# Kernel tuning notes

Hardware: AMD Instinct MI355X
Metric: run time of the kernel (lower is better)

Reference implementation:

```python
import jax, jax.numpy as jnp
import numpy as np

NEG_INF = -1e30  # stand-in for float('-inf') that is softmax-safe


def setup_inputs() -> dict:
    key = jax.random.key(0)
    ks = jax.random.split(key, 6)
    B, H, S, D = 2, 8, 1024, 64
    NF, K = 4, 3
    return {
        "query": jax.random.normal(ks[0], (B, H, S, D), dtype=jnp.float32),
        "keys": jax.random.normal(ks[1], (B, H, S, D), dtype=jnp.float32),
        "vals": jax.random.normal(ks[2], (B, H, S, D), dtype=jnp.float32),
        "mask": jnp.ones((B, 1, S, S), dtype=jnp.int32),
        "conv_w": jax.random.normal(ks[3], (NF, 1, K, K), dtype=jnp.float32) * (1.0 / K),
        "conv_b": jnp.zeros((NF,), dtype=jnp.float32),
        "lin_w": jax.random.normal(ks[4], (1, NF), dtype=jnp.float32) * 0.5,
        "lin_b": jnp.zeros((1,), dtype=jnp.float32),
    }


def reference(query, keys, vals, mask, conv_w, conv_b, lin_w, lin_b):
    B, H, S, D = query.shape
    NF = conv_w.shape[0]
    K = conv_w.shape[2]
    scale = jnp.asarray(D, query.dtype) ** 0.5

    # [B,H,S,S] raw dot-product scores
    dp = jnp.einsum("bhsd,bhtd->bhst", query, keys) / scale

    # conv2d over the score matrix: treat (B*H) as batch, 1 input channel
    x = dp.reshape(B * H, 1, S, S)
    conv = jax.lax.conv_general_dilated(
        x, conv_w,
        window_strides=(1, 1),
        padding=[(K // 2, K // 2), (K // 2, K // 2)],
        dimension_numbers=("NCHW", "OIHW", "NCHW"),
    ) + conv_b[None, :, None, None]
    conv = jax.nn.leaky_relu(conv, negative_slope=0.01)  # [B*H, NF, S, S]

    # per-pixel linear over the filter axis (Linear(num_filters, 1))
    conv = conv.reshape(B, H, NF, S, S)
    preattn = jnp.einsum("bhfst,f->bhst", conv, lin_w[0]) + lin_b[0]

    # masking + softmax (mask broadcasts over heads)
    preattn = jnp.where(mask == 0, jnp.asarray(NEG_INF, preattn.dtype), preattn)
    attn = jax.nn.softmax(preattn, axis=-1)

    # dropout is identity in eval mode
    return jnp.einsum("bhst,bhtd->bhsd", attn, vals)
```

## Files before the change

kernel.cpp:

```cpp
#include <hip/hip_runtime.h>
#include <math.h>

#define S_LEN 1024
#define D_DIM 64
#define NBH   16
#define RPB   14
#define NSB   74

typedef unsigned short ushort_t;
typedef unsigned int uint_t;
typedef __attribute__((ext_vector_type(8))) _Float16 half8;
typedef __attribute__((ext_vector_type(2))) _Float16 h2;
typedef __attribute__((ext_vector_type(4))) short short4v;
typedef __attribute__((ext_vector_type(4))) float f32x4;

__device__ __forceinline__ ushort_t f16bits(float x) {
    _Float16 h = (_Float16)x;
    ushort_t b;
    __builtin_memcpy(&b, &h, 2);
    return b;
}
__device__ __forceinline__ h2 as_h2(uint_t u) {
    h2 r;
    __builtin_memcpy(&r, &u, 4);
    return r;
}
__device__ __forceinline__ float uniform_f(float x) {
    return __int_as_float(__builtin_amdgcn_readfirstlane(__float_as_int(x)));
}
__device__ __forceinline__ float fast_exp2(float x) {
#if __has_builtin(__builtin_amdgcn_exp2f)
    return __builtin_amdgcn_exp2f(x);
#else
    return exp2f(x);
#endif
}

__global__ __launch_bounds__(256) void prep(
    const float* __restrict__ k, const float* __restrict__ v,
    const int* __restrict__ mask,
    ushort_t* __restrict__ kh, ushort_t* __restrict__ vh,
    unsigned* __restrict__ mw)
{
    __shared__ float Ls[64][65];
    const int tid = threadIdx.x;
    const int bx = blockIdx.x;
    if (bx < 512) {
        const int gid  = bx * 256 + tid;
        const int bh   = gid >> 13;
        const int tile = (gid >> 7) & 63;
        const int ch   = (gid >> 6) & 1;
        const int lane = gid & 63;
        const int quad = lane >> 4, t15 = lane & 15;
        const float* src = k + ((size_t)bh * S_LEN + tile * 16 + t15) * D_DIM
                             + ch * 32 + quad * 8;
        float x[8];
        *(float4*)(x + 0) = *(const float4*)(src);
        *(float4*)(x + 4) = *(const float4*)(src + 4);
        ushort_t hv[8];
        #pragma unroll
        for (int i = 0; i < 8; ++i) hv[i] = f16bits(x[i] * 0.125f);
        *(short4v*)(kh + (size_t)gid * 8)     = *(short4v*)(hv);
        *(short4v*)(kh + (size_t)gid * 8 + 4) = *(short4v*)(hv + 4);
    } else if (bx < 768) {
        const int bi = bx - 512;
        const int tt = bi & 15, bh = bi >> 4;
        const float* vb = v + ((size_t)bh * S_LEN + tt * 64) * D_DIM;
        #pragma unroll
        for (int p = 0; p < 4; ++p) {
            int idx = p * 1024 + tid * 4;
            int r = idx >> 6, c = idx & 63;
            float4 x = *(const float4*)(vb + r * 64 + c);
            Ls[r][c] = x.x; Ls[r][c+1] = x.y; Ls[r][c+2] = x.z; Ls[r][c+3] = x.w;
        }
        __syncthreads();
        const int d = tid >> 2, c0 = (tid & 3) * 16;
        ushort_t hi[16];
        #pragma unroll
        for (int j = 0; j < 16; ++j) hi[j] = f16bits(Ls[c0 + j][d]);
        const int tb0 = tt * 8 + (c0 >> 3);
        const size_t o0 = (((size_t)bh * 128 + tb0) * 64 + d) * 8;
        const size_t o1 = (((size_t)bh * 128 + tb0 + 1) * 64 + d) * 8;
        *(short4v*)(vh + o0)     = *(short4v*)(hi);
        *(short4v*)(vh + o0 + 4) = *(short4v*)(hi + 4);
        *(short4v*)(vh + o1)     = *(short4v*)(hi + 8);
        *(short4v*)(vh + o1 + 4) = *(short4v*)(hi + 12);
    } else {
        const int gid = (bx - 768) * 256 + tid;
        const int row = gid >> 5, wd = gid & 31;
        const int4* mp = (const int4*)(mask + (size_t)row * 1024 + wd * 32);
        unsigned bits = 0;
        #pragma unroll
        for (int p = 0; p < 8; ++p) {
            int4 qv = mp[p];
            bits |= (qv.x != 0 ? 1u : 0u) << (p * 4 + 0);
            bits |= (qv.y != 0 ? 1u : 0u) << (p * 4 + 1);
            bits |= (qv.z != 0 ? 1u : 0u) << (p * 4 + 2);
            bits |= (qv.w != 0 ? 1u : 0u) << (p * 4 + 3);
        }
        mw[(size_t)row * 32 + wd] = bits;
    }
}

#define DPSTR 1040
__global__ __launch_bounds__(512) void fused_qk_conv_av(
    const float* __restrict__ q,
    const ushort_t* __restrict__ kh, const unsigned* __restrict__ mw,
    const ushort_t* __restrict__ vh,
    const float* __restrict__ conv_w, const float* __restrict__ conv_b,
    const float* __restrict__ lin_w, const float* __restrict__ lin_b,
    float* __restrict__ out)
{
    __shared__ ushort_t dpH[16 * DPSTR];
    __shared__ float oBuf[16][68];
    __shared__ float lsRow[16];
    __shared__ unsigned mb[16][32];

    const int st = blockIdx.x, bh = blockIdx.y;
    const int s0 = st * RPB;
    const int b  = bh >> 3;
    const int tid = threadIdx.x;
    const int wave = tid >> 6, lane = tid & 63;
    const int m = lane & 15, quad = lane >> 4;

    {
        const int o = tid >> 5, wd = tid & 31;
        const int s = s0 - 1 + o;
        mb[o][wd] = (s >= 0 && s < S_LEN)
                  ? mw[((size_t)b * S_LEN + s) * 32 + wd] : 0u;
    }
    if (tid < 64) {
        const int row = tid >> 2, i = tid & 3;
        const int idx = (i < 2) ? i : 1024 + i;
        dpH[row * DPSTR + idx] = 0;
    }

    const int sA = s0 - 1 + m;
    const int sQ = sA < 0 ? 0 : (sA > S_LEN - 1 ? S_LEN - 1 : sA);
    const float* qp = q + ((size_t)bh * S_LEN + sQ) * D_DIM + quad * 8;
    float qa[16];
    *(float4*)(qa + 0)  = *(const float4*)(qp + 0);
    *(float4*)(qa + 4)  = *(const float4*)(qp + 4);
    *(float4*)(qa + 8)  = *(const float4*)(qp + 32);
    *(float4*)(qa + 12) = *(const float4*)(qp + 36);
    half8 AH0, AH1;
    #pragma unroll
    for (int i = 0; i < 8; ++i) {
        AH0[i] = (_Float16)qa[i];
        AH1[i] = (_Float16)qa[8 + i];
    }

    #pragma unroll
    for (int tt = 0; tt < 8; ++tt) {
        const int tile = wave * 8 + tt;
        const size_t kb = (((size_t)bh * 64 + tile) * 128 + lane) * 8;
        half8 KH0 = *(const half8*)(kh + kb);
        half8 KH1 = *(const half8*)(kh + kb + 512);
        f32x4 a = {0.f, 0.f, 0.f, 0.f};
        a = __builtin_amdgcn_mfma_f32_16x16x32_f16(AH0, KH0, a, 0, 0, 0);
        a = __builtin_amdgcn_mfma_f32_16x16x32_f16(AH1, KH1, a, 0, 0, 0);
        const int col = tile * 16 + m;
        #pragma unroll
        for (int r = 0; r < 4; ++r) {
            const int row = quad * 4 + r;
            const int s = s0 - 1 + row;
            const float v = (s >= 0 && s < S_LEN) ? a[r] : 0.f;
            dpH[row * DPSTR + col + 2] = f16bits(v);
        }
    }

    float w[36];
    #pragma unroll
    for (int i = 0; i < 36; ++i) w[i] = conv_w[i];
    const float L2E = 1.44269504088896341f;
    float cb[4], aF[4], bF[4];
    #pragma unroll
    for (int f = 0; f < 4; ++f) {
        cb[f] = conv_b[f];
        const float lwf = lin_w[f];
        aF[f] = uniform_f(0.505f * lwf * L2E);
        bF[f] = uniform_f(0.495f * lwf * L2E);
    }
    const float lbE = uniform_f(lin_b[0] * L2E);

    __syncthreads();

    const int rh = tid >> 8, cg = tid & 255, c0 = cg * 4;
    uint2 Ps[8];
    #pragma unroll
    for (int pass = 0; pass < 2; ++pass) {
        const int obase = rh * 8 + pass * 4;
        float xv[6][6];
        #pragma unroll
        for (int jj = 0; jj < 6; ++jj) {
            const int dr = obase - 1 + jj;
            if (dr >= 0 && dr < 16) {
                const ushort_t* rp = &dpH[dr * DPSTR + c0];
                uint2 r0 = *(const uint2*)rp;
                uint2 r1 = *(const uint2*)(rp + 4);
                h2 pA = as_h2(r0.x), pB = as_h2(r0.y);
                h2 pC = as_h2(r1.x), pD = as_h2(r1.y);
                xv[jj][0] = (float)pA[1];
                xv[jj][1] = (float)pB[0]; xv[jj][2] = (float)pB[1];
                xv[jj][3] = (float)pC[0]; xv[jj][4] = (float)pC[1];
                xv[jj][5] = (float)pD[0];
            } else {
                #pragma unroll
                for (int i = 0; i < 6; ++i) xv[jj][i] = 0.f;
            }
        }
        #pragma unroll
        for (int jo = 0; jo < 4; ++jo) {
            const int o = obase + jo;
            const bool act = (o >= 1) && (o <= RPB) && (s0 - 1 + o < S_LEN);
            if (act) {
                float pr[4] = {lbE, lbE, lbE, lbE};
                #pragma unroll
                for (int f = 0; f < 4; ++f) {
                    const float* wf = w + f * 9;
                    float acc[4];
                    const float w00 = wf[0];
                    #pragma unroll
                    for (int c = 0; c < 4; ++c) acc[c] = w00 * xv[jo][c];
                    #pragma unroll
                    for (int t = 1; t < 9; ++t) {
                        const int dr = t / 3, dc = t % 3;
                        const float wt = wf[t];
                        #pragma unroll
                        for (int c = 0; c < 4; ++c)
                            acc[c] = fmaf(wt, xv[jo + dr][dc + c], acc[c]);
                    }
                    const float cbf = cb[f], af = aF[f], bf = bF[f];
                    #pragma unroll
                    for (int c = 0; c < 4; ++c) {
                        const float y = acc[c] + cbf;
                        pr[c] = fmaf(af, y, pr[c]);
                        pr[c] = fmaf(bf, fabsf(y), pr[c]);
                    }
                }
                const unsigned word = mb[o][cg >> 3];
                const unsigned nib  = (word >> ((cg & 7) * 4)) & 0xFu;
                float pv[4];
                #pragma unroll
                for (int c = 0; c < 4; ++c) {
                    const float pe = ((nib >> c) & 1u) ? pr[c] : -1e30f;
                    pv[c] = fast_exp2(pe);
                }
                Ps[pass * 4 + jo].x =
                    (uint_t)f16bits(pv[0]) | ((uint_t)f16bits(pv[1]) << 16);
                Ps[pass * 4 + jo].y =
                    (uint_t)f16bits(pv[2]) | ((uint_t)f16bits(pv[3]) << 16);
            } else {
                Ps[pass * 4 + jo].x = 0u;
                Ps[pass * 4 + jo].y = 0u;
            }
        }
    }
    __syncthreads();

    #pragma unroll
    for (int i = 0; i < 8; ++i) {
        const int o = rh * 8 + i;
        *(uint2*)&dpH[o * DPSTR + c0] = Ps[i];
    }
    __syncthreads();

    const int d0 = (wave & 3) * 16;
    const int th = wave >> 2;
    f32x4 O  = {0.f, 0.f, 0.f, 0.f};
    f32x4 RS = {0.f, 0.f, 0.f, 0.f};
    half8 ONE;
    #pragma unroll
    for (int i = 0; i < 8; ++i) ONE[i] = (_Float16)1.0f;
    const ushort_t* ph_base = &dpH[m * DPSTR + th * 512 + quad * 8];
    const ushort_t* vv_base = vh + ((size_t)bh * 65536
                                    + (size_t)(th * 64 + quad) * 512
                                    + (size_t)(d0 + m) * 8);
    #pragma unroll 4
    for (int i = 0; i < 16; ++i) {
        half8 ph = *(const half8*)(ph_base + i * 32);
        half8 vv = *(const half8*)(vv_base + (size_t)i * 2048);
        O  = __builtin_amdgcn_mfma_f32_16x16x32_f16(ph, vv, O, 0, 0, 0);
        RS = __builtin_amdgcn_mfma_f32_16x16x32_f16(ph, ONE, RS, 0, 0, 0);
    }
    if (wave < 4) {
        #pragma unroll
        for (int r = 0; r < 4; ++r) oBuf[quad * 4 + r][d0 + m] = O[r];
    }
    if (wave == 0 && m == 0) {
        #pragma unroll
        for (int r = 0; r < 4; ++r) lsRow[quad * 4 + r] = RS[r];
    }
    __syncthreads();
    if (wave >= 4) {
        #pragma unroll
        for (int r = 0; r < 4; ++r) {
            const int br = quad * 4 + r;
            const int s = s0 - 1 + br;
            if (br >= 1 && br <= RPB && s < S_LEN) {
                const float lsum = lsRow[br] + RS[r];
                out[((size_t)bh * S_LEN + s) * D_DIM + d0 + m] =
                    (O[r] + oBuf[br][d0 + m]) / lsum;
            }
        }
    }
}

extern "C" void kernel_launch(void* const* d_in, const int* in_sizes, int n_in,
                              void* d_out, int out_size, void* d_ws, size_t ws_size,
                              hipStream_t stream) {
    const float* q      = (const float*)d_in[0];
    const float* k      = (const float*)d_in[1];
    const float* v      = (const float*)d_in[2];
    const int*   mask   = (const int*)d_in[3];
    const float* conv_w = (const float*)d_in[4];
    const float* conv_b = (const float*)d_in[5];
    const float* lin_w  = (const float*)d_in[6];
    const float* lin_b  = (const float*)d_in[7];
    float* out = (float*)d_out;

    char* wsb = (char*)d_ws;
    const size_t MB = 1024 * 1024;
    ushort_t* kh = (ushort_t*)(wsb + 0 * MB);
    ushort_t* vh = (ushort_t*)(wsb + 2 * MB);
    unsigned* mw = (unsigned*)(wsb + 4 * MB);

    prep<<<dim3(1024), 256, 0, stream>>>(k, v, mask, kh, vh, mw);
    fused_qk_conv_av<<<dim3(NSB, NBH), 512, 0, stream>>>(
        q, kh, mw, vh, conv_w, conv_b, lin_w, lin_b, out);
}
```

Before: 117.3 us.

## Compute 3x3 conv over score tile with MFMA using banded weight matrices

```diff
diff --git a/kernel.cpp b/kernel.cpp
--- a/kernel.cpp
+++ b/kernel.cpp
@@ -20,11 +20,6 @@
     __builtin_memcpy(&b, &h, 2);
     return b;
 }
-__device__ __forceinline__ h2 as_h2(uint_t u) {
-    h2 r;
-    __builtin_memcpy(&r, &u, 4);
-    return r;
-}
 __device__ __forceinline__ float uniform_f(float x) {
     return __int_as_float(__builtin_amdgcn_readfirstlane(__float_as_int(x)));
 }
@@ -35,12 +30,18 @@
     return exp2f(x);
 #endif
 }
+__device__ __forceinline__ half8 ld_half8_b64(const ushort_t* p) {
+    union { uint2 u[2]; half8 h; } c;
+    c.u[0] = *(const uint2*)p;
+    c.u[1] = *(const uint2*)(p + 4);
+    return c.h;
+}
 
 __global__ __launch_bounds__(256) void prep(
     const float* __restrict__ k, const float* __restrict__ v,
-    const int* __restrict__ mask,
+    const int* __restrict__ mask, const float* __restrict__ conv_w,
     ushort_t* __restrict__ kh, ushort_t* __restrict__ vh,
-    unsigned* __restrict__ mw)
+    unsigned* __restrict__ mw, ushort_t* __restrict__ wtab)
 {
     __shared__ float Ls[64][65];
     const int tid = threadIdx.x;
@@ -85,7 +86,7 @@
         *(short4v*)(vh + o0 + 4) = *(short4v*)(hi + 4);
         *(short4v*)(vh + o1)     = *(short4v*)(hi + 8);
         *(short4v*)(vh + o1 + 4) = *(short4v*)(hi + 12);
-    } else {
+    } else if (bx < 1024) {
         const int gid = (bx - 768) * 256 + tid;
         const int row = gid >> 5, wd = gid & 31;
         const int4* mp = (const int4*)(mask + (size_t)row * 1024 + wd * 32);
@@ -99,22 +100,58 @@
             bits |= (qv.w != 0 ? 1u : 0u) << (p * 4 + 3);
         }
         mw[(size_t)row * 32 + wd] = bits;
-    }
-}
-
-#define DPSTR 1040
+    } else {
+        if (tid < 64) {
+            const int o = tid & 15, qd = tid >> 4;
+            half8* wt = (half8*)wtab;
+            #pragma unroll
+            for (int f = 0; f < 4; ++f) {
+                half8 fr0 = {}, fr1 = {}, fr2 = {};
+                #pragma unroll
+                for (int i = 0; i < 8; ++i) {
+                    const int kk = qd * 8 + i;
+                    const int r  = kk & 15;
+                    const bool hiK = kk < 16;
+                    #pragma unroll
+                    for (int dr = 0; dr < 3; ++dr) {
+                        if (r - o == dr - 1) {
+                            const float w0 = conv_w[f*9 + dr*3 + 0];
+                            const float w1 = conv_w[f*9 + dr*3 + 1];
+                            const float w2 = conv_w[f*9 + dr*3 + 2];
+                            const _Float16 w0h = (_Float16)w0;
+                            const _Float16 w1h = (_Float16)w1;
+                            const _Float16 w2h = (_Float16)w2;
+                            const _Float16 w0l = (_Float16)(w0 - (float)w0h);
+                            const _Float16 w1l = (_Float16)(w1 - (float)w1h);
+                            const _Float16 w2l = (_Float16)(w2 - (float)w2h);
+                            fr0[i] = hiK ? w0h : w1h;
+                            fr1[i] = hiK ? w0l : w1l;
+                            fr2[i] = hiK ? w2h : w2l;
+                        }
+                    }
+                }
+                wt[(f*3 + 0) * 64 + tid] = fr0;
+                wt[(f*3 + 1) * 64 + tid] = fr1;
+                wt[(f*3 + 2) * 64 + tid] = fr2;
+            }
+        }
+    }
+}
+
+#define DPTSTR 20
+#define PSTR   1048
 __global__ __launch_bounds__(512) void fused_qk_conv_av(
     const float* __restrict__ q,
     const ushort_t* __restrict__ kh, const unsigned* __restrict__ mw,
-    const ushort_t* __restrict__ vh,
-    const float* __restrict__ conv_w, const float* __restrict__ conv_b,
+    const ushort_t* __restrict__ vh, const ushort_t* __restrict__ wtab,
+    const float* __restrict__ conv_b,
     const float* __restrict__ lin_w, const float* __restrict__ lin_b,
     float* __restrict__ out)
 {
-    __shared__ ushort_t dpH[16 * DPSTR];
+    __shared__ ushort_t sBuf[1028 * DPTSTR];
     __shared__ float oBuf[16][68];
     __shared__ float lsRow[16];
-    __shared__ unsigned mb[16][32];
+    __shared__ unsigned mbT[32][16];
 
     const int st = blockIdx.x, bh = blockIdx.y;
     const int s0 = st * RPB;
@@ -123,16 +160,25 @@
     const int wave = tid >> 6, lane = tid & 63;
     const int m = lane & 15, quad = lane >> 4;
 
+    half8 WF[4][3];
     {
-        const int o = tid >> 5, wd = tid & 31;
+        const half8* wt = (const half8*)wtab;
+        #pragma unroll
+        for (int f = 0; f < 4; ++f)
+            #pragma unroll
+            for (int g = 0; g < 3; ++g)
+                WF[f][g] = wt[(f*3 + g) * 64 + lane];
+    }
+
+    {
+        const int wd = tid >> 4, o = tid & 15;
         const int s = s0 - 1 + o;
-        mb[o][wd] = (s >= 0 && s < S_LEN)
-                  ? mw[((size_t)b * S_LEN + s) * 32 + wd] : 0u;
-    }
-    if (tid < 64) {
-        const int row = tid >> 2, i = tid & 3;
-        const int idx = (i < 2) ? i : 1024 + i;
-        dpH[row * DPSTR + idx] = 0;
+        mbT[wd][o] = (s >= 0 && s < S_LEN)
+                   ? mw[((size_t)b * S_LEN + s) * 32 + wd] : 0u;
+    }
+    if (tid < 32) {
+        const int row = (tid < 16) ? 1 : 1026;
+        sBuf[row * DPTSTR + (tid & 15)] = 0;
     }
 
     const int sA = s0 - 1 + m;
@@ -159,19 +205,19 @@
         f32x4 a = {0.f, 0.f, 0.f, 0.f};
         a = __builtin_amdgcn_mfma_f32_16x16x32_f16(AH0, KH0, a, 0, 0, 0);
         a = __builtin_amdgcn_mfma_f32_16x16x32_f16(AH1, KH1, a, 0, 0, 0);
-        const int col = tile * 16 + m;
+        ushort_t t4[4];
         #pragma unroll
         for (int r = 0; r < 4; ++r) {
-            const int row = quad * 4 + r;
-            const int s = s0 - 1 + row;
+            const int s = s0 - 1 + quad * 4 + r;
             const float v = (s >= 0 && s < S_LEN) ? a[r] : 0.f;
-            dpH[row * DPSTR + col + 2] = f16bits(v);
-        }
-    }
-
-    float w[36];
-    #pragma unroll
-    for (int i = 0; i < 36; ++i) w[i] = conv_w[i];
+            t4[r] = f16bits(v);
+        }
+        uint2 wv2;
+        wv2.x = (uint_t)t4[0] | ((uint_t)t4[1] << 16);
+        wv2.y = (uint_t)t4[2] | ((uint_t)t4[3] << 16);
+        *(uint2*)&sBuf[(tile * 16 + m + 2) * DPTSTR + quad * 4] = wv2;
+    }
+
     const float L2E = 1.44269504088896341f;
     float cb[4], aF[4], bF[4];
     #pragma unroll
@@ -185,83 +231,58 @@
 
     __syncthreads();
 
-    const int rh = tid >> 8, cg = tid & 255, c0 = cg * 4;
-    uint2 Ps[8];
-    #pragma unroll
-    for (int pass = 0; pass < 2; ++pass) {
-        const int obase = rh * 8 + pass * 4;
-        float xv[6][6];
-        #pragma unroll
-        for (int jj = 0; jj < 6; ++jj) {
-            const int dr = obase - 1 + jj;
-            if (dr >= 0 && dr < 16) {
-                const ushort_t* rp = &dpH[dr * DPSTR + c0];
-                uint2 r0 = *(const uint2*)rp;
-                uint2 r1 = *(const uint2*)(rp + 4);
-                h2 pA = as_h2(r0.x), pB = as_h2(r0.y);
-                h2 pC = as_h2(r1.x), pD = as_h2(r1.y);
-                xv[jj][0] = (float)pA[1];
-                xv[jj][1] = (float)pB[0]; xv[jj][2] = (float)pB[1];
-                xv[jj][3] = (float)pC[0]; xv[jj][4] = (float)pC[1];
-                xv[jj][5] = (float)pD[0];
-            } else {
-                #pragma unroll
-                for (int i = 0; i < 6; ++i) xv[jj][i] = 0.f;
+    const int i01 = (m + 1 + (quad >> 1)) * DPTSTR + (quad & 1) * 8
+                  + wave * (8 * 16 * DPTSTR);
+    const int i22 = (m + 3) * DPTSTR + (quad & 1) * 8
+                  + wave * (8 * 16 * DPTSTR);
+    uint_t Ps[16];
+    #pragma unroll
+    for (int tt = 0; tt < 8; ++tt) {
+        const int tile = wave * 8 + tt;
+        half8 B01 = ld_half8_b64(&sBuf[i01 + tt * (16 * DPTSTR)]);
+        half8 B22 = ld_half8_b64(&sBuf[i22 + tt * (16 * DPTSTR)]);
+        f32x4 acc[4];
+        #pragma unroll
+        for (int f = 0; f < 4; ++f) {
+            const float cbf = cb[f];
+            acc[f] = (f32x4){cbf, cbf, cbf, cbf};
+            acc[f] = __builtin_amdgcn_mfma_f32_16x16x32_f16(WF[f][0], B01, acc[f], 0, 0, 0);
+            acc[f] = __builtin_amdgcn_mfma_f32_16x16x32_f16(WF[f][1], B01, acc[f], 0, 0, 0);
+            acc[f] = __builtin_amdgcn_mfma_f32_16x16x32_f16(WF[f][2], B22, acc[f], 0, 0, 0);
+        }
+        const uint4 mq = *(const uint4*)&mbT[tile >> 1][quad * 4];
+        const int cbit = ((tile & 1) << 4) + m;
+        float pv[4];
+        #pragma unroll
+        for (int r = 0; r < 4; ++r) {
+            const int o = quad * 4 + r;
+            const bool act = (o >= 1) && (o <= RPB) && (s0 - 1 + o < S_LEN);
+            float pre = lbE;
+            #pragma unroll
+            for (int f = 0; f < 4; ++f) {
+                const float y = acc[f][r];
+                pre = fmaf(aF[f], y, pre);
+                pre = fmaf(bF[f], fabsf(y), pre);
             }
-        }
-        #pragma unroll
-        for (int jo = 0; jo < 4; ++jo) {
-            const int o = obase + jo;
-            const bool act = (o >= 1) && (o <= RPB) && (s0 - 1 + o < S_LEN);
-            if (act) {
-                float pr[4] = {lbE, lbE, lbE, lbE};
-                #pragma unroll
-                for (int f = 0; f < 4; ++f) {
-                    const float* wf = w + f * 9;
-                    float acc[4];
-                    const float w00 = wf[0];
-                    #pragma unroll
-                    for (int c = 0; c < 4; ++c) acc[c] = w00 * xv[jo][c];
-                    #pragma unroll
-                    for (int t = 1; t < 9; ++t) {
-                        const int dr = t / 3, dc = t % 3;
-                        const float wt = wf[t];
-                        #pragma unroll
-                        for (int c = 0; c < 4; ++c)
-                            acc[c] = fmaf(wt, xv[jo + dr][dc + c], acc[c]);
-                    }
-                    const float cbf = cb[f], af = aF[f], bf = bF[f];
-                    #pragma unroll
-                    for (int c = 0; c < 4; ++c) {
-                        const float y = acc[c] + cbf;
-                        pr[c] = fmaf(af, y, pr[c]);
-                        pr[c] = fmaf(bf, fabsf(y), pr[c]);
-                    }
-                }
-                const unsigned word = mb[o][cg >> 3];
-                const unsigned nib  = (word >> ((cg & 7) * 4)) & 0xFu;
-                float pv[4];
-                #pragma unroll
-                for (int c = 0; c < 4; ++c) {
-                    const float pe = ((nib >> c) & 1u) ? pr[c] : -1e30f;
-                    pv[c] = fast_exp2(pe);
-                }
-                Ps[pass * 4 + jo].x =
-                    (uint_t)f16bits(pv[0]) | ((uint_t)f16bits(pv[1]) << 16);
-                Ps[pass * 4 + jo].y =
-                    (uint_t)f16bits(pv[2]) | ((uint_t)f16bits(pv[3]) << 16);
-            } else {
-                Ps[pass * 4 + jo].x = 0u;
-                Ps[pass * 4 + jo].y = 0u;
-            }
-        }
+            const unsigned mword = (r == 0) ? mq.x : (r == 1) ? mq.y
+                                 : (r == 2) ? mq.z : mq.w;
+            const bool keep = act && ((mword >> cbit) & 1u);
+            pv[r] = fast_exp2(keep ? pre : -1e30f);
+        }
+        Ps[2*tt + 0] = (uint_t)f16bits(pv[0]) | ((uint_t)f16bits(pv[1]) << 16);
+        Ps[2*tt + 1] = (uint_t)f16bits(pv[2]) | ((uint_t)f16bits(pv[3]) << 16);
     }
     __syncthreads();
 
     #pragma unroll
-    for (int i = 0; i < 8; ++i) {
-        const int o = rh * 8 + i;
-        *(uint2*)&dpH[o * DPSTR + c0] = Ps[i];
+    for (int tt = 0; tt < 8; ++tt) {
+        const int c = (wave * 8 + tt) * 16 + m;
+        ushort_t* pp = &sBuf[quad * 4 * PSTR + c];
+        const uint_t lo = Ps[2*tt], hi = Ps[2*tt + 1];
+        pp[0]        = (ushort_t)lo;
+        pp[PSTR]     = (ushort_t)(lo >> 16);
+        pp[2*PSTR]   = (ushort_t)hi;
+        pp[3*PSTR]   = (ushort_t)(hi >> 16);
     }
     __syncthreads();
 
@@ -272,7 +293,7 @@
     half8 ONE;
     #pragma unroll
     for (int i = 0; i < 8; ++i) ONE[i] = (_Float16)1.0f;
-    const ushort_t* ph_base = &dpH[m * DPSTR + th * 512 + quad * 8];
+    const ushort_t* ph_base = &sBuf[m * PSTR + th * 512 + quad * 8];
     const ushort_t* vv_base = vh + ((size_t)bh * 65536
                                     + (size_t)(th * 64 + quad) * 512
                                     + (size_t)(d0 + m) * 8);
@@ -321,11 +342,12 @@
 
     char* wsb = (char*)d_ws;
     const size_t MB = 1024 * 1024;
-    ushort_t* kh = (ushort_t*)(wsb + 0 * MB);
-    ushort_t* vh = (ushort_t*)(wsb + 2 * MB);
-    unsigned* mw = (unsigned*)(wsb + 4 * MB);
-
-    prep<<<dim3(1024), 256, 0, stream>>>(k, v, mask, kh, vh, mw);
+    ushort_t* kh   = (ushort_t*)(wsb + 0 * MB);
+    ushort_t* vh   = (ushort_t*)(wsb + 2 * MB);
+    unsigned* mw   = (unsigned*)(wsb + 4 * MB);
+    ushort_t* wtab = (ushort_t*)(wsb + 4 * MB + 256 * 1024);
+
+    prep<<<dim3(1025), 256, 0, stream>>>(k, v, mask, conv_w, kh, vh, mw, wtab);
     fused_qk_conv_av<<<dim3(NSB, NBH), 512, 0, stream>>>(
-        q, kh, mw, vh, conv_w, conv_b, lin_w, lin_b, out);
-}
+        q, kh, mw, vh, wtab, conv_b, lin_w, lin_b, out);
+}
```

Measured after the change: 130.5 us. 11.3% more time.
